# Kernel optimization log

Hardware: AMD Instinct MI355X
Metric: run time of the kernel (lower is better)

The kernel has to match this reference:

```python
import jax, jax.numpy as jnp
import numpy as np

N_NODES = 100000
N_EDGES = 1600000
HID = 128
N_CONV = 3  # num_layers - 1
OUT_DIM = 1
BN_EPS = 1e-5


def _batchnorm(z, gamma, beta):
    # training-mode BN over node dim (batch statistics, biased variance)
    mean = jnp.mean(z, axis=0)
    var = jnp.mean((z - mean) ** 2, axis=0)
    return (z - mean) * jax.lax.rsqrt(var + BN_EPS) * gamma + beta


def setup_inputs() -> dict:
    key = jax.random.key(0)
    ks = jax.random.split(key, 16)
    s = 0.05
    inp = {
        "x": jax.random.randint(ks[0], (N_NODES,), 0, 2, dtype=jnp.int32),
        "edge_index": jax.random.randint(ks[1], (2, N_EDGES), 0, N_NODES, dtype=jnp.int64),
        "emb": jax.random.normal(ks[2], (2, HID), jnp.float32) * s,
        "W1": jax.random.normal(ks[3], (N_CONV, HID, HID), jnp.float32) * s,
        "W2": jax.random.normal(ks[4], (N_CONV, HID, HID), jnp.float32) * s,
        "bn1_g": jnp.ones((N_CONV, HID), jnp.float32),
        "bn1_b": jnp.zeros((N_CONV, HID), jnp.float32),
        "bn2_g": jnp.ones((N_CONV, HID), jnp.float32),
        "bn2_b": jnp.zeros((N_CONV, HID), jnp.float32),
        "rW1": jax.random.normal(ks[5], (4 * HID, HID), jnp.float32) * s,
        "rb1": jnp.zeros((HID,), jnp.float32),
        "rW2": jax.random.normal(ks[6], (HID, OUT_DIM), jnp.float32) * s,
        "rb2": jnp.zeros((OUT_DIM,), jnp.float32),
    }
    return inp


def reference(x, edge_index, emb, W1, W2, bn1_g, bn1_b, bn2_g, bn2_b, rW1, rb1, rW2, rb2):
    n = x.shape[0]
    src, dst = edge_index[0], edge_index[1]
    h = emb[x]  # [N, HID]
    reps = [h]
    for i in range(N_CONV):
        # GINConv: mlp((1+eps)*h + sum_{j in N(i)} h_j), eps=0
        agg = jax.ops.segment_sum(h[src], dst, num_segments=n)
        z = h + agg
        z = jnp.einsum('nd,df->nf', z, W1[i])
        z = jax.nn.relu(_batchnorm(z, bn1_g[i], bn1_b[i]))
        z = jnp.einsum('nd,df->nf', z, W2[i])
        z = _batchnorm(z, bn2_g[i], bn2_b[i])  # PyG BatchNorm after conv
        h = jax.nn.elu(z)
        reps.append(h)
    cat = jnp.concatenate(reps, axis=-1)  # [N, 4*HID]
    hid = jax.nn.relu(cat @ rW1 + rb1)
    return hid @ rW2 + rb2  # [N, OUT_DIM]
```

## Files before the change

kernel.cpp:

```cpp
#include <hip/hip_runtime.h>
#include <hip/hip_fp16.h>
#include <cstdint>
#include <cstddef>

#define NN 100000
#define NE 1600000
#define HID 128
#define BN_EPS 1e-5f
#define NB_SCAN 98
#define BM 96
#define NBLK ((NN + BM - 1) / BM)
#define NBC  ((NN + 255) / 256)
#define SA 72
#define SC_CHUNKS 256
#define SC_RANGE (NN / 8)
#define SC_EPC (NE / SC_CHUNKS)

typedef __attribute__((ext_vector_type(8))) short bf16x8;
typedef __attribute__((ext_vector_type(8))) _Float16 f16x8;
typedef __attribute__((ext_vector_type(4))) float f32x4;
typedef __attribute__((ext_vector_type(4))) unsigned short u16x4;

static constexpr size_t SZ_NODE = (size_t)NN * HID * 4;
static constexpr size_t SZ_H16  = (size_t)NN * HID * 2;
static constexpr size_t OFF_P   = 0;
static constexpr size_t OFF_Q   = SZ_NODE;
static constexpr size_t OFF_R   = 2 * SZ_NODE;
static constexpr size_t OFF_CSR = 3 * SZ_NODE;
static constexpr size_t OFF_RP  = OFF_CSR + (size_t)NE * 4;
static constexpr size_t OFF_ZZ  = ((OFF_RP + (size_t)(NN + 1) * 4 + 255) / 256) * 256;
static constexpr size_t OFF_CNT = OFF_ZZ;
static constexpr size_t OFF_BS  = OFF_CNT + (((size_t)NN * 4 + 255) / 256) * 256;
static constexpr size_t OFF_FLG = OFF_BS + 512;
static constexpr size_t OFF_SS  = OFF_FLG + 256;
static constexpr size_t OFF_SCT = OFF_SS + 5 * 256 * 4;
static constexpr size_t ZZ_END  = ((OFF_SCT + 5 * 4 + 255) / 256) * 256;
static constexpr size_t ZZ_BYTES = ZZ_END - OFF_ZZ;
static constexpr size_t OFF_AC  = ZZ_END;
static constexpr size_t OFF_E   = OFF_AC + 6 * 256 * 4;
static constexpr size_t OFF_WSP = OFF_E + 512 * 4;
static constexpr size_t WS_NEEDED = OFF_WSP + (size_t)8 * 2 * HID * HID * 2;

__device__ __forceinline__ unsigned short f2bf(float f) {
  unsigned u = __float_as_uint(f);
  unsigned r = (u + 0x7fffu + ((u >> 16) & 1u)) >> 16;
  return (unsigned short)r;
}
__device__ __forceinline__ float bf2f(unsigned short b) {
  return __uint_as_float(((unsigned)b) << 16);
}
__device__ __forceinline__ int edge_at(const int* __restrict__ E, int f, int idx) {
  return f ? E[2 * (long long)idx] : E[idx];
}

__global__ void k_detect(const int* __restrict__ E, int* __restrict__ flag) {
  if (threadIdx.x == 0 && blockIdx.x == 0) {
    int f = 1;
    for (int i = 1; i < 256; i += 2)
      if (E[i] != 0) { f = 0; break; }
    *flag = f;
  }
}

__global__ __launch_bounds__(256) void k_hist(const int* __restrict__ E,
                                              const int* __restrict__ flag,
                                              int* __restrict__ cnt) {
  const int f = *flag;
  const int r = blockIdx.x & 7;
  const int chunk = blockIdx.x >> 3;
  const int lo = r * SC_RANGE, hi = lo + SC_RANGE;
  const int ebeg = chunk * SC_EPC, eend = ebeg + SC_EPC;
  for (int e = ebeg + threadIdx.x; e < eend; e += 256) {
    int d = edge_at(E, f, NE + e);
    d = min(max(d, 0), NN - 1);
    if (d >= lo && d < hi) atomicAdd(&cnt[d], 1);
  }
}

__global__ __launch_bounds__(256) void k_scan1(const int* __restrict__ cnt,
                                               int* __restrict__ rp,
                                               int* __restrict__ bs) {
  __shared__ int s[256];
  const int tid = threadIdx.x;
  const int base = blockIdx.x * 1024 + tid * 4;
  int v0 = 0, v1 = 0, v2 = 0, v3 = 0;
  if (base + 0 < NN) v0 = cnt[base + 0];
  if (base + 1 < NN) v1 = cnt[base + 1];
  if (base + 2 < NN) v2 = cnt[base + 2];
  if (base + 3 < NN) v3 = cnt[base + 3];
  const int t0 = v0, t1 = t0 + v1, t2 = t1 + v2, t3 = t2 + v3;
  s[tid] = t3;
  __syncthreads();
  for (int off = 1; off < 256; off <<= 1) {
    int xv = 0;
    if (tid >= off) xv = s[tid - off];
    __syncthreads();
    if (tid >= off) s[tid] += xv;
    __syncthreads();
  }
  const int excl = tid ? s[tid - 1] : 0;
  if (base + 0 < NN) rp[base + 0] = excl;
  if (base + 1 < NN) rp[base + 1] = excl + t0;
  if (base + 2 < NN) rp[base + 2] = excl + t1;
  if (base + 3 < NN) rp[base + 3] = excl + t2;
  if (tid == 255) bs[blockIdx.x] = s[255];
}

__global__ __launch_bounds__(128) void k_scan2(int* __restrict__ bs) {
  __shared__ int s[128];
  const int tid = threadIdx.x;
  s[tid] = (tid < NB_SCAN) ? bs[tid] : 0;
  __syncthreads();
  for (int off = 1; off < 128; off <<= 1) {
    int xv = 0;
    if (tid >= off) xv = s[tid - off];
    __syncthreads();
    if (tid >= off) s[tid] += xv;
    __syncthreads();
  }
  if (tid < NB_SCAN) bs[tid] = tid ? s[tid - 1] : 0;
}

__global__ __launch_bounds__(256) void k_scan3(int* __restrict__ rp,
                                               const int* __restrict__ bs,
                                               int* __restrict__ cursor) {
  const int off = bs[blockIdx.x];
  const int base = blockIdx.x * 1024 + threadIdx.x * 4;
  #pragma unroll
  for (int j = 0; j < 4; ++j) {
    const int i = base + j;
    if (i < NN) {
      const int v = rp[i] + off;
      rp[i] = v;
      cursor[i] = v;
    }
  }
  if (blockIdx.x == 0 && threadIdx.x == 0) rp[NN] = NE;
}

__global__ __launch_bounds__(256) void k_scatter(const int* __restrict__ E,
                                                 const int* __restrict__ flag,
                                                 const int* __restrict__ x,
                                                 int* __restrict__ cursor,
                                                 int* __restrict__ csr) {
  const int f = *flag;
  const int r = blockIdx.x & 7;
  const int chunk = blockIdx.x >> 3;
  const int lo = r * SC_RANGE, hi = lo + SC_RANGE;
  const int ebeg = chunk * SC_EPC, eend = ebeg + SC_EPC;
  for (int e = ebeg + threadIdx.x; e < eend; e += 256) {
    int d = edge_at(E, f, NE + e);
    d = min(max(d, 0), NN - 1);
    if (d >= lo && d < hi) {
      int s = edge_at(E, f, e);
      s = min(max(s, 0), NN - 1);
      const int xb = x[s] & 1;
      const int pos = atomicAdd(&cursor[d], 1);
      if ((unsigned)pos < (unsigned)NE) csr[pos] = s | (xb << 31);
    }
  }
}

__global__ __launch_bounds__(256) void k_prepw(const float* __restrict__ W1,
                                               const float* __restrict__ W2,
                                               const float* __restrict__ rW1,
                                               short* __restrict__ wsp) {
  const int g = blockIdx.x * 256 + threadIdx.x;
  const int m = g >> 14, idx = g & 16383;
  const int k = idx >> 7, n = idx & 127;
  const float* src;
  switch (m) {
    case 0: src = W2; break;
    case 1: src = W1 + 1 * HID * HID; break;
    case 2: src = W2 + 1 * HID * HID; break;
    case 3: src = W1 + 2 * HID * HID; break;
    case 4: src = W2 + 2 * HID * HID; break;
    case 5: src = rW1 + 1 * HID * HID; break;
    case 6: src = rW1 + 2 * HID * HID; break;
    default: src = rW1 + 3 * HID * HID; break;
  }
  const float v = src[k * HID + n];
  short* dst = wsp + (size_t)m * 32768;
  if (m < 5) {
    const unsigned short hb = f2bf(v);
    dst[n * HID + k] = (short)hb;
    dst[16384 + n * HID + k] = (short)f2bf(v - bf2f(hb));
  } else {
    const __half hh = __float2half_rn(v);
    const float rem = v - __half2float(hh);
    const __half hl = __float2half_rn(rem * 2048.f);
    dst[n * HID + k] = (short)__half_as_ushort(hh);
    dst[16384 + n * HID + k] = (short)__half_as_ushort(hl);
  }
}

__global__ __launch_bounds__(256) void k_prep(const float* __restrict__ emb,
                                              const float* __restrict__ W1,
                                              const float* __restrict__ rW1,
                                              float* __restrict__ ee) {
  const int t = threadIdx.x;
  const int f = t & 127;
  const float* er = emb + (t >> 7) * HID;
  float se = 0.f, sr = 0.f;
  for (int k = 0; k < HID; ++k) {
    const float ev = er[k];
    se = fmaf(ev, W1[k * HID + f], se);
    sr = fmaf(ev, rW1[k * HID + f], sr);
  }
  ee[t] = se;
  ee[256 + t] = sr;
}

__global__ __launch_bounds__(256) void k_cnt(const int* __restrict__ x,
                                             const int* __restrict__ rp,
                                             const int* __restrict__ csr,
                                             int* __restrict__ a01,
                                             float* __restrict__ momp) {
  const int n = blockIdx.x * 256 + threadIdx.x;
  float m[5] = {0.f, 0.f, 0.f, 0.f, 0.f};
  if (n < NN) {
    const int beg = rp[n], end = rp[n + 1];
    int c1 = 0;
    for (int j = beg; j < end; ++j) c1 += (int)(((unsigned)csr[j]) >> 31);
    const int a1 = c1 + (x[n] & 1);
    const int a0 = (end - beg + 1) - a1;
    a01[n] = a0 | (a1 << 16);
    m[0] = (float)a0;
    m[1] = (float)a1;
    m[2] = (float)a0 * (float)a0;
    m[3] = (float)a1 * (float)a1;
    m[4] = (float)a0 * (float)a1;
  }
  #pragma unroll
  for (int j = 0; j < 5; ++j)
    #pragma unroll
    for (int off = 1; off < 64; off <<= 1) m[j] += __shfl_xor(m[j], off);
  __shared__ float sm[5][4];
  const int lane = threadIdx.x & 63, wv = threadIdx.x >> 6;
  if (lane == 0)
    #pragma unroll
    for (int j = 0; j < 5; ++j) sm[j][wv] = m[j];
  __syncthreads();
  if (threadIdx.x == 0)
    #pragma unroll
    for (int j = 0; j < 5; ++j)
      momp[j * NBC + blockIdx.x] = sm[j][0] + sm[j][1] + sm[j][2] + sm[j][3];
}

__global__ __launch_bounds__(128) void k_bnmom(const float* __restrict__ momp,
                                               const float* __restrict__ ee,
                                               const float* __restrict__ g,
                                               const float* __restrict__ b,
                                               float* __restrict__ a,
                                               float* __restrict__ c) {
  __shared__ float red[5][128];
  const int t = threadIdx.x;
  float s[5] = {0.f, 0.f, 0.f, 0.f, 0.f};
  for (int i = t; i < NBC; i += 128)
    #pragma unroll
    for (int j = 0; j < 5; ++j) s[j] += momp[j * NBC + i];
  #pragma unroll
  for (int j = 0; j < 5; ++j) red[j][t] = s[j];
  __syncthreads();
  for (int off = 64; off; off >>= 1) {
    if (t < off)
      #pragma unroll
      for (int j = 0; j < 5; ++j) red[j][t] += red[j][t + off];
    __syncthreads();
  }
  const float S0 = red[0][0], S1 = red[1][0];
  const float S00 = red[2][0], S11 = red[3][0], S01 = red[4][0];
  const float inv_n = 1.0f / (float)NN;
  const float e0 = ee[t], e1 = ee[128 + t];
  const float mean = (S0 * e0 + S1 * e1) * inv_n;
  const float msq = (S00 * e0 * e0 + 2.f * S01 * e0 * e1 + S11 * e1 * e1) * inv_n;
  float var = fmaxf(msq - mean * mean, 0.f);
  const float rs = rsqrtf(var + BN_EPS);
  const float av = g[t] * rs;
  a[t] = av;
  c[t] = b[t] - mean * av;
}

__global__ __launch_bounds__(256) void k_agg(const __half* __restrict__ h,
                                             const int* __restrict__ rp,
                                             const int* __restrict__ csr,
                                             float* __restrict__ z) {
  const int wid = blockIdx.x * 4 + (threadIdx.x >> 6);
  const int lane = threadIdx.x & 63;
  if (wid >= NN) return;
  const int beg = rp[wid], end = rp[wid + 1];
  float2 acc = __half22float2(*((const __half2*)(h + (size_t)wid * HID) + lane));
  for (int j = beg; j < end; j += 64) {
    const int cnt = min(64, end - j);
    int idx = (lane < cnt) ? (csr[j + lane] & 0x7fffffff) : 0;
    idx = min(idx, NN - 1);
    int k = 0;
    for (; k + 4 <= cnt; k += 4) {
      const int s0 = __shfl(idx, k + 0), s1 = __shfl(idx, k + 1);
      const int s2 = __shfl(idx, k + 2), s3 = __shfl(idx, k + 3);
      const float2 v0 = __half22float2(*((const __half2*)(h + (size_t)s0 * HID) + lane));
      const float2 v1 = __half22float2(*((const __half2*)(h + (size_t)s1 * HID) + lane));
      const float2 v2 = __half22float2(*((const __half2*)(h + (size_t)s2 * HID) + lane));
      const float2 v3 = __half22float2(*((const __half2*)(h + (size_t)s3 * HID) + lane));
      acc.x += (v0.x + v1.x) + (v2.x + v3.x);
      acc.y += (v0.y + v1.y) + (v2.y + v3.y);
    }
    for (; k < cnt; ++k) {
      const int s = __shfl(idx, k);
      const float2 v = __half22float2(*((const __half2*)(h + (size_t)s * HID) + lane));
      acc.x += v.x;
      acc.y += v.y;
    }
  }
  *(float2*)(z + (size_t)wid * HID + lane * 2) = acc;
}

template <int IN_ACT, int OUT_MODE>
__global__ __launch_bounds__(256, 4) void k_gemm(
    float* A, const short* __restrict__ Wsp,
    const float* __restrict__ ina, const float* __restrict__ inc,
    float* __restrict__ out, float* __restrict__ part,
    const int* __restrict__ a01, const float* __restrict__ ee) {
  __shared__ short Ah[BM * SA];
  __shared__ short Al[BM * SA];
  const int tid = threadIdx.x;
  const int lane = tid & 63, wv = tid >> 6;
  const int tq = lane >> 4, tl = lane & 15;
  const int wc = wv * 32;
  const int m0 = blockIdx.x * BM;

  f32x4 acc[6][2];
  #pragma unroll
  for (int i = 0; i < 6; ++i)
    #pragma unroll
    for (int j = 0; j < 2; ++j) acc[i][j] = (f32x4)(0.f);

  for (int kt = 0; kt < HID; kt += 64) {
    if (kt) __syncthreads();
    #pragma unroll
    for (int p = 0; p < 6; ++p) {
      const int flat = p * 256 + tid;
      const int m = flat >> 4, kq = flat & 15;
      const int gm = m0 + m, gk = kt + kq * 4;
      float vv[4] = {0.f, 0.f, 0.f, 0.f};
      if (gm < NN) {
        if (IN_ACT == 2) {
          const int pk = a01[gm];
          const float a0 = (float)(pk & 0xffff), a1 = (float)(pk >> 16);
          const float4 e0q = *(const float4*)(ee + gk);
          const float4 e1q = *(const float4*)(ee + 128 + gk);
          vv[0] = a0 * e0q.x + a1 * e1q.x;
          vv[1] = a0 * e0q.y + a1 * e1q.y;
          vv[2] = a0 * e0q.z + a1 * e1q.z;
          vv[3] = a0 * e0q.w + a1 * e1q.w;
        } else {
          const float4 v = *(const float4*)(A + (size_t)gm * HID + gk);
          vv[0] = v.x; vv[1] = v.y; vv[2] = v.z; vv[3] = v.w;
        }
        if (IN_ACT >= 1) {
          const float4 a4 = *(const float4*)(ina + gk);
          const float4 c4 = *(const float4*)(inc + gk);
          vv[0] = fmaxf(fmaf(vv[0], a4.x, c4.x), 0.f);
          vv[1] = fmaxf(fmaf(vv[1], a4.y, c4.y), 0.f);
          vv[2] = fmaxf(fmaf(vv[2], a4.z, c4.z), 0.f);
          vv[3] = fmaxf(fmaf(vv[3], a4.w, c4.w), 0.f);
        }
      }
      u16x4 hh, ll;
      #pragma unroll
      for (int j = 0; j < 4; ++j) {
        const unsigned short hb = f2bf(vv[j]);
        hh[j] = hb;
        ll[j] = f2bf(vv[j] - bf2f(hb));
      }
      *(u16x4*)(&Ah[m * SA + kq * 4]) = hh;
      *(u16x4*)(&Al[m * SA + kq * 4]) = ll;
    }
    __syncthreads();
    #pragma unroll
    for (int kc = 0; kc < 64; kc += 32) {
      const int lo = kc + tq * 8;
      const int go = kt + lo;
      bf16x8 wh[2], wl[2];
      #pragma unroll
      for (int fn = 0; fn < 2; ++fn) {
        const int n = wc + fn * 16 + tl;
        wh[fn] = *(const bf16x8*)(Wsp + n * HID + go);
        wl[fn] = *(const bf16x8*)(Wsp + 16384 + n * HID + go);
      }
      #pragma unroll
      for (int fm = 0; fm < 6; ++fm) {
        const int r = (fm * 16 + tl) * SA + lo;
        const bf16x8 ah = *(const bf16x8*)(&Ah[r]);
        const bf16x8 al = *(const bf16x8*)(&Al[r]);
        #pragma unroll
        for (int fn = 0; fn < 2; ++fn) {
          acc[fm][fn] = __builtin_amdgcn_mfma_f32_16x16x32_bf16(ah, wh[fn], acc[fm][fn], 0, 0, 0);
          acc[fm][fn] = __builtin_amdgcn_mfma_f32_16x16x32_bf16(ah, wl[fn], acc[fm][fn], 0, 0, 0);
          acc[fm][fn] = __builtin_amdgcn_mfma_f32_16x16x32_bf16(al, wh[fn], acc[fm][fn], 0, 0, 0);
        }
      }
    }
  }

  #pragma unroll
  for (int fm = 0; fm < 6; ++fm) {
    #pragma unroll
    for (int reg = 0; reg < 4; ++reg) {
      const int row = m0 + fm * 16 + tq * 4 + reg;
      if (row < NN) {
        float* op = out + (size_t)row * HID + wc + tl;
        op[0] = acc[fm][0][reg];
        op[16] = acc[fm][1][reg];
      }
    }
  }
  if (OUT_MODE == 0) {
    #pragma unroll
    for (int fn = 0; fn < 2; ++fn) {
      float s = 0.f, q = 0.f;
      #pragma unroll
      for (int fm = 0; fm < 6; ++fm)
        #pragma unroll
        for (int reg = 0; reg < 4; ++reg) {
          const float v = acc[fm][fn][reg];
          s += v;
          q = fmaf(v, v, q);
        }
      s += __shfl_xor(s, 16); q += __shfl_xor(q, 16);
      s += __shfl_xor(s, 32); q += __shfl_xor(q, 32);
      if (lane < 16) {
        const int col = wc + fn * 16 + lane;
        part[(size_t)blockIdx.x * 256 + col] = s;
        part[(size_t)blockIdx.x * 256 + 128 + col] = q;
      }
    }
  }
}

__global__ __launch_bounds__(256, 3) void k_rdgemm(
    const __half* __restrict__ h1, const __half* __restrict__ h2,
    const __half* __restrict__ h3, const short* __restrict__ wsp,
    const int* __restrict__ x, const float* __restrict__ ee,
    const float* __restrict__ rb1, const float* __restrict__ rW2,
    const float* __restrict__ rb2, float* __restrict__ out) {
  __shared__ short Ah[BM * SA];
  const int tid = threadIdx.x;
  const int lane = tid & 63, wv = tid >> 6;
  const int tq = lane >> 4, tl = lane & 15;
  const int wc = wv * 32;
  const int m0 = blockIdx.x * BM;

  f32x4 ach[6][2], acl[6][2];
  #pragma unroll
  for (int i = 0; i < 6; ++i)
    #pragma unroll
    for (int j = 0; j < 2; ++j) { ach[i][j] = (f32x4)(0.f); acl[i][j] = (f32x4)(0.f); }

  for (int t6 = 0; t6 < 6; ++t6) {
    const __half* hsrc = (t6 < 2) ? h1 : (t6 < 4) ? h2 : h3;
    const short* Ws = wsp + (size_t)(t6 >> 1) * 32768;
    const int kt = (t6 & 1) * 64;
    if (t6) __syncthreads();
    #pragma unroll
    for (int p = 0; p < 6; ++p) {
      const int flat = p * 256 + tid;
      const int m = flat >> 4, kq = flat & 15;
      const int gm = m0 + m, gk = kt + kq * 4;
      u16x4 hv = (u16x4)(0);
      if (gm < NN) hv = *(const u16x4*)((const unsigned short*)hsrc + (size_t)gm * HID + gk);
      *(u16x4*)(&Ah[m * SA + kq * 4]) = hv;
    }
    __syncthreads();
    #pragma unroll
    for (int kc = 0; kc < 64; kc += 32) {
      const int lo = kc + tq * 8;
      const int go = kt + lo;
      f16x8 wh[2], wl[2];
      #pragma unroll
      for (int fn = 0; fn < 2; ++fn) {
        const int n = wc + fn * 16 + tl;
        wh[fn] = *(const f16x8*)(Ws + n * HID + go);
        wl[fn] = *(const f16x8*)(Ws + 16384 + n * HID + go);
      }
      #pragma unroll
      for (int fm = 0; fm < 6; ++fm) {
        const f16x8 a = *(const f16x8*)(&Ah[(fm * 16 + tl) * SA + lo]);
        #pragma unroll
        for (int fn = 0; fn < 2; ++fn) {
          ach[fm][fn] = __builtin_amdgcn_mfma_f32_16x16x32_f16(a, wh[fn], ach[fm][fn], 0, 0, 0);
          acl[fm][fn] = __builtin_amdgcn_mfma_f32_16x16x32_f16(a, wl[fn], acl[fm][fn], 0, 0, 0);
        }
      }
    }
  }

  const int c0 = wc + tl, c1 = wc + 16 + tl;
  const float rb_0 = rb1[c0], rb_1 = rb1[c1];
  const float w2_0 = rW2[c0], w2_1 = rW2[c1];
  const float r0_0 = ee[256 + c0], r0_1 = ee[256 + c1];
  const float r1_0 = ee[384 + c0], r1_1 = ee[384 + c1];
  const float LS = 1.0f / 2048.0f;
  __syncthreads();
  float* rs = (float*)Ah;
  #pragma unroll
  for (int fm = 0; fm < 6; ++fm) {
    #pragma unroll
    for (int reg = 0; reg < 4; ++reg) {
      const int row = fm * 16 + tq * 4 + reg;
      const int grow = m0 + row;
      const int xv = (grow < NN) ? (x[grow] & 1) : 0;
      const float g0 = ach[fm][0][reg] + acl[fm][0][reg] * LS + rb_0 + (xv ? r1_0 : r0_0);
      const float g1 = ach[fm][1][reg] + acl[fm][1][reg] * LS + rb_1 + (xv ? r1_1 : r0_1);
      float p = fmaxf(g0, 0.f) * w2_0 + fmaxf(g1, 0.f) * w2_1;
      p += __shfl_xor(p, 1);
      p += __shfl_xor(p, 2);
      p += __shfl_xor(p, 4);
      p += __shfl_xor(p, 8);
      if (tl == 0) rs[row * 4 + wv] = p;
    }
  }
  __syncthreads();
  if (tid < BM) {
    const int grow = m0 + tid;
    if (grow < NN)
      out[grow] = rs[tid * 4 + 0] + rs[tid * 4 + 1] + rs[tid * 4 + 2] +
                  rs[tid * 4 + 3] + rb2[0];
  }
}

__global__ __launch_bounds__(256) void k_bnstat(const float* __restrict__ part,
                                                const float* __restrict__ g,
                                                const float* __restrict__ b,
                                                float* __restrict__ a,
                                                float* __restrict__ c,
                                                float* __restrict__ S,
                                                int* __restrict__ ctr) {
  const int tid = threadIdx.x;
  float acc = 0.f;
  for (int r = blockIdx.x; r < NBLK; r += 64) acc += part[(size_t)r * 256 + tid];
  atomicAdd(&S[tid], acc);
  __syncthreads();
  __threadfence();
  __shared__ int last;
  if (tid == 0) last = (atomicAdd(ctr, 1) == 63);
  __syncthreads();
  if (!last) return;
  __threadfence();
  const float tot = atomicAdd(&S[tid], 0.f);
  __shared__ float sm[256];
  sm[tid] = tot;
  __syncthreads();
  if (tid < 128) {
    const float inv_n = 1.0f / (float)NN;
    const float mean = sm[tid] * inv_n;
    float var = fmaxf(sm[tid + 128] * inv_n - mean * mean, 0.f);
    const float rs = rsqrtf(var + BN_EPS);
    const float av = g[tid] * rs;
    a[tid] = av;
    c[tid] = b[tid] - mean * av;
  }
}

__global__ __launch_bounds__(256) void k_act(const float* __restrict__ v,
                                             const float* __restrict__ a,
                                             const float* __restrict__ c,
                                             __half* __restrict__ h) {
  const int total = NN * 32;
  for (int i = blockIdx.x * blockDim.x + threadIdx.x; i < total;
       i += gridDim.x * blockDim.x) {
    const int node = i >> 5, q = i & 31;
    const float4 vv = *(const float4*)(v + (size_t)node * HID + q * 4);
    const float4 a4 = ((const float4*)a)[q];
    const float4 c4 = ((const float4*)c)[q];
    float z;
    float o0, o1, o2, o3;
    z = fmaf(vv.x, a4.x, c4.x); o0 = z > 0.f ? z : expm1f(z);
    z = fmaf(vv.y, a4.y, c4.y); o1 = z > 0.f ? z : expm1f(z);
    z = fmaf(vv.z, a4.z, c4.z); o2 = z > 0.f ? z : expm1f(z);
    z = fmaf(vv.w, a4.w, c4.w); o3 = z > 0.f ? z : expm1f(z);
    const __half2 p0 = __floats2half2_rn(o0, o1);
    const __half2 p1 = __floats2half2_rn(o2, o3);
    uint2 u;
    u.x = *reinterpret_cast<const unsigned*>(&p0);
    u.y = *reinterpret_cast<const unsigned*>(&p1);
    *(uint2*)(h + (size_t)node * HID + q * 4) = u;
  }
}

extern "C" void kernel_launch(void* const* d_in, const int* in_sizes, int n_in,
                              void* d_out, int out_size, void* d_ws,
                              size_t ws_size, hipStream_t stream) {
  if (ws_size < WS_NEEDED) return;

  const int* x = (const int*)d_in[0];
  const int* E = (const int*)d_in[1];
  const float* emb = (const float*)d_in[2];
  const float* W1 = (const float*)d_in[3];
  const float* W2 = (const float*)d_in[4];
  const float* bn1g = (const float*)d_in[5];
  const float* bn1b = (const float*)d_in[6];
  const float* bn2g = (const float*)d_in[7];
  const float* bn2b = (const float*)d_in[8];
  const float* rW1 = (const float*)d_in[9];
  const float* rb1 = (const float*)d_in[10];
  const float* rW2 = (const float*)d_in[11];
  const float* rb2 = (const float*)d_in[12];
  float* outp = (float*)d_out;

  char* ws = (char*)d_ws;
  float* P = (float*)(ws + OFF_P);
  float* Q = (float*)(ws + OFF_Q);
  float* R = (float*)(ws + OFF_R);
  int* csr = (int*)(ws + OFF_CSR);
  int* rp = (int*)(ws + OFF_RP);
  int* cnt = (int*)(ws + OFF_CNT);
  int* bs = (int*)(ws + OFF_BS);
  int* flag = (int*)(ws + OFF_FLG);
  float* SS = (float*)(ws + OFF_SS);
  int* SCT = (int*)(ws + OFF_SCT);
  float* ac = (float*)(ws + OFF_AC);
  float* ee = (float*)(ws + OFF_E);
  short* wsp = (short*)(ws + OFF_WSP);
  __half* h1 = (__half*)P;
  __half* h2 = (__half*)((char*)P + SZ_H16);
  __half* h3 = (__half*)R;
  float* part = R;
  int* a01 = (int*)((char*)P + (4 << 20));
  float* momp = (float*)((char*)P + (8 << 20));

  hipMemsetAsync(ws + OFF_ZZ, 0, ZZ_BYTES, stream);
  k_detect<<<1, 64, 0, stream>>>(E, flag);
  k_hist<<<SC_CHUNKS * 8, 256, 0, stream>>>(E, flag, cnt);
  k_scan1<<<NB_SCAN, 256, 0, stream>>>(cnt, rp, bs);
  k_scan2<<<1, 128, 0, stream>>>(bs);
  k_scan3<<<NB_SCAN, 256, 0, stream>>>(rp, bs, cnt);
  k_scatter<<<SC_CHUNKS * 8, 256, 0, stream>>>(E, flag, x, cnt, csr);
  k_prep<<<1, 256, 0, stream>>>(emb, W1, rW1, ee);
  k_prepw<<<512, 256, 0, stream>>>(W1, W2, rW1, wsp);

  float* a1 = ac + 0 * 256, *c1 = a1 + HID;
  float* a2 = ac + 1 * 256, *c2 = a2 + HID;

  k_cnt<<<NBC, 256, 0, stream>>>(x, rp, csr, a01, momp);
  k_bnmom<<<1, 128, 0, stream>>>(momp, ee, bn1g, bn1b, a1, c1);
  k_gemm<2, 0><<<NBLK, 256, 0, stream>>>(Q, wsp + 0 * 32768, a1, c1, Q, part,
                                         a01, ee);
  k_bnstat<<<64, 256, 0, stream>>>(part, bn2g, bn2b, a2, c2, SS + 0 * 256, SCT + 0);
  k_act<<<2048, 256, 0, stream>>>(Q, a2, c2, h1);

  int inst = 1;
  for (int i = 1; i < 3; ++i) {
    float* b1a = ac + (2 * i) * 256, *b1c = b1a + HID;
    float* b2a = ac + (2 * i + 1) * 256, *b2c = b2a + HID;
    const int s1 = (i == 1) ? 1 : 3;
    const __half* hin = (i == 1) ? h1 : h2;
    k_agg<<<NN / 4, 256, 0, stream>>>(hin, rp, csr, Q);
    k_gemm<0, 0><<<NBLK, 256, 0, stream>>>(Q, wsp + (size_t)s1 * 32768,
                                           nullptr, nullptr, Q, part, nullptr,
                                           nullptr);
    k_bnstat<<<64, 256, 0, stream>>>(part, bn1g + i * HID, bn1b + i * HID, b1a,
                                     b1c, SS + inst * 256, SCT + inst);
    ++inst;
    k_gemm<1, 0><<<NBLK, 256, 0, stream>>>(Q, wsp + (size_t)(s1 + 1) * 32768,
                                           b1a, b1c, Q, part, nullptr, nullptr);
    k_bnstat<<<64, 256, 0, stream>>>(part, bn2g + i * HID, bn2b + i * HID, b2a,
                                     b2c, SS + inst * 256, SCT + inst);
    ++inst;
    k_act<<<2048, 256, 0, stream>>>(Q, b2a, b2c, (i == 1) ? h2 : h3);
  }

  k_rdgemm<<<NBLK, 256, 0, stream>>>(h1, h2, h3, wsp + (size_t)5 * 32768, x, ee,
                                     rb1, rW2, rb2, outp);
}
```

Measured before the change: 710.1 us.

## Rewrite GEMMs to load activations straight into registers, dropping LDS staging

The node-level GEMM and readout GEMM kernels are restructured. Each wave now owns 32 rows and all 128 output columns, and reads its A fragments directly from global memory into MFMA registers. This removes the LDS staging and the block-wide barriers. Per-block column statistics are reduced through a small shared buffer. The readout GEMM also drops the low-order fp16 weight correction term and its extra MFMAs, which costs some precision in the final MLP. The trade-off is more weight traffic per wave and lower accuracy in the readout.

New measurement: 819.1 us. 15.3% more time.

```diff
diff --git a/kernel.cpp b/kernel.cpp
--- a/kernel.cpp
+++ b/kernel.cpp
@@ -8,10 +8,9 @@
 #define HID 128
 #define BN_EPS 1e-5f
 #define NB_SCAN 98
-#define BM 96
-#define NBLK ((NN + BM - 1) / BM)
+#define BM2 128
+#define NBLK2 ((NN + BM2 - 1) / BM2)
 #define NBC  ((NN + 255) / 256)
-#define SA 72
 #define SC_CHUNKS 256
 #define SC_RANGE (NN / 8)
 #define SC_EPC (NE / SC_CHUNKS)
@@ -19,7 +18,6 @@
 typedef __attribute__((ext_vector_type(8))) short bf16x8;
 typedef __attribute__((ext_vector_type(8))) _Float16 f16x8;
 typedef __attribute__((ext_vector_type(4))) float f32x4;
-typedef __attribute__((ext_vector_type(4))) unsigned short u16x4;
 
 static constexpr size_t SZ_NODE = (size_t)NN * HID * 4;
 static constexpr size_t SZ_H16  = (size_t)NN * HID * 2;
@@ -187,10 +185,8 @@
     dst[16384 + n * HID + k] = (short)f2bf(v - bf2f(hb));
   } else {
     const __half hh = __float2half_rn(v);
-    const float rem = v - __half2float(hh);
-    const __half hl = __float2half_rn(rem * 2048.f);
     dst[n * HID + k] = (short)__half_as_ushort(hh);
-    dst[16384 + n * HID + k] = (short)__half_as_ushort(hl);
+    dst[16384 + n * HID + k] = 0;
   }
 }
 
@@ -315,217 +311,213 @@
   *(float2*)(z + (size_t)wid * HID + lane * 2) = acc;
 }
 
-template <int IN_ACT, int OUT_MODE>
-__global__ __launch_bounds__(256, 4) void k_gemm(
-    float* A, const short* __restrict__ Wsp,
+template <int IN_ACT>
+__global__ __launch_bounds__(256, 4) void k_gemm2(
+    const float* __restrict__ A, const short* __restrict__ Wsp,
     const float* __restrict__ ina, const float* __restrict__ inc,
     float* __restrict__ out, float* __restrict__ part,
     const int* __restrict__ a01, const float* __restrict__ ee) {
-  __shared__ short Ah[BM * SA];
-  __shared__ short Al[BM * SA];
+  __shared__ float red[4][256];
   const int tid = threadIdx.x;
   const int lane = tid & 63, wv = tid >> 6;
   const int tq = lane >> 4, tl = lane & 15;
-  const int wc = wv * 32;
-  const int m0 = blockIdx.x * BM;
-
-  f32x4 acc[6][2];
-  #pragma unroll
-  for (int i = 0; i < 6; ++i)
-    #pragma unroll
-    for (int j = 0; j < 2; ++j) acc[i][j] = (f32x4)(0.f);
-
-  for (int kt = 0; kt < HID; kt += 64) {
-    if (kt) __syncthreads();
-    #pragma unroll
-    for (int p = 0; p < 6; ++p) {
-      const int flat = p * 256 + tid;
-      const int m = flat >> 4, kq = flat & 15;
-      const int gm = m0 + m, gk = kt + kq * 4;
-      float vv[4] = {0.f, 0.f, 0.f, 0.f};
-      if (gm < NN) {
-        if (IN_ACT == 2) {
-          const int pk = a01[gm];
-          const float a0 = (float)(pk & 0xffff), a1 = (float)(pk >> 16);
-          const float4 e0q = *(const float4*)(ee + gk);
-          const float4 e1q = *(const float4*)(ee + 128 + gk);
-          vv[0] = a0 * e0q.x + a1 * e1q.x;
-          vv[1] = a0 * e0q.y + a1 * e1q.y;
-          vv[2] = a0 * e0q.z + a1 * e1q.z;
-          vv[3] = a0 * e0q.w + a1 * e1q.w;
-        } else {
-          const float4 v = *(const float4*)(A + (size_t)gm * HID + gk);
-          vv[0] = v.x; vv[1] = v.y; vv[2] = v.z; vv[3] = v.w;
-        }
-        if (IN_ACT >= 1) {
-          const float4 a4 = *(const float4*)(ina + gk);
-          const float4 c4 = *(const float4*)(inc + gk);
-          vv[0] = fmaxf(fmaf(vv[0], a4.x, c4.x), 0.f);
-          vv[1] = fmaxf(fmaf(vv[1], a4.y, c4.y), 0.f);
-          vv[2] = fmaxf(fmaf(vv[2], a4.z, c4.z), 0.f);
-          vv[3] = fmaxf(fmaf(vv[3], a4.w, c4.w), 0.f);
-        }
-      }
-      u16x4 hh, ll;
+  const int rw = blockIdx.x * BM2 + wv * 32;
+
+  f32x4 acc[2][8];
+  #pragma unroll
+  for (int i = 0; i < 2; ++i)
+    #pragma unroll
+    for (int j = 0; j < 8; ++j) acc[i][j] = (f32x4)(0.f);
+
+  int a01r[2] = {0, 0};
+  if (IN_ACT == 2) {
+    a01r[0] = a01[min(rw + tl, NN - 1)];
+    a01r[1] = a01[min(rw + 16 + tl, NN - 1)];
+  }
+
+  #pragma unroll
+  for (int ks = 0; ks < 4; ++ks) {
+    const int kg = ks * 32 + tq * 8;
+    float aa[8], cc[8];
+    if (IN_ACT >= 1) {
+      const float4 a0 = *(const float4*)(ina + kg);
+      const float4 a1 = *(const float4*)(ina + kg + 4);
+      const float4 c0 = *(const float4*)(inc + kg);
+      const float4 c1 = *(const float4*)(inc + kg + 4);
+      aa[0] = a0.x; aa[1] = a0.y; aa[2] = a0.z; aa[3] = a0.w;
+      aa[4] = a1.x; aa[5] = a1.y; aa[6] = a1.z; aa[7] = a1.w;
+      cc[0] = c0.x; cc[1] = c0.y; cc[2] = c0.z; cc[3] = c0.w;
+      cc[4] = c1.x; cc[5] = c1.y; cc[6] = c1.z; cc[7] = c1.w;
+    }
+    float e0v[8], e1v[8];
+    if (IN_ACT == 2) {
+      const float4 p0 = *(const float4*)(ee + kg);
+      const float4 p1 = *(const float4*)(ee + kg + 4);
+      const float4 q0 = *(const float4*)(ee + 128 + kg);
+      const float4 q1 = *(const float4*)(ee + 128 + kg + 4);
+      e0v[0] = p0.x; e0v[1] = p0.y; e0v[2] = p0.z; e0v[3] = p0.w;
+      e0v[4] = p1.x; e0v[5] = p1.y; e0v[6] = p1.z; e0v[7] = p1.w;
+      e1v[0] = q0.x; e1v[1] = q0.y; e1v[2] = q0.z; e1v[3] = q0.w;
+      e1v[4] = q1.x; e1v[5] = q1.y; e1v[6] = q1.z; e1v[7] = q1.w;
+    }
+    bf16x8 ah[2], al[2];
+    #pragma unroll
+    for (int fm = 0; fm < 2; ++fm) {
+      const int row = rw + fm * 16 + tl;
+      const int rc = min(row, NN - 1);
+      float vv[8];
+      if (IN_ACT == 2) {
+        const float b0 = (float)(a01r[fm] & 0xffff);
+        const float b1 = (float)(a01r[fm] >> 16);
+        #pragma unroll
+        for (int j = 0; j < 8; ++j) vv[j] = b0 * e0v[j] + b1 * e1v[j];
+      } else {
+        const float4 v0 = *(const float4*)(A + (size_t)rc * HID + kg);
+        const float4 v1 = *(const float4*)(A + (size_t)rc * HID + kg + 4);
+        vv[0] = v0.x; vv[1] = v0.y; vv[2] = v0.z; vv[3] = v0.w;
+        vv[4] = v1.x; vv[5] = v1.y; vv[6] = v1.z; vv[7] = v1.w;
+      }
+      if (IN_ACT >= 1) {
+        #pragma unroll
+        for (int j = 0; j < 8; ++j) vv[j] = fmaxf(fmaf(vv[j], aa[j], cc[j]), 0.f);
+      }
+      if (row >= NN) {
+        #pragma unroll
+        for (int j = 0; j < 8; ++j) vv[j] = 0.f;
+      }
       #pragma unroll
-      for (int j = 0; j < 4; ++j) {
+      for (int j = 0; j < 8; ++j) {
         const unsigned short hb = f2bf(vv[j]);
-        hh[j] = hb;
-        ll[j] = f2bf(vv[j] - bf2f(hb));
-      }
-      *(u16x4*)(&Ah[m * SA + kq * 4]) = hh;
-      *(u16x4*)(&Al[m * SA + kq * 4]) = ll;
-    }
-    __syncthreads();
-    #pragma unroll
-    for (int kc = 0; kc < 64; kc += 32) {
-      const int lo = kc + tq * 8;
-      const int go = kt + lo;
-      bf16x8 wh[2], wl[2];
+        ah[fm][j] = (short)hb;
+        al[fm][j] = (short)f2bf(vv[j] - bf2f(hb));
+      }
+    }
+    #pragma unroll
+    for (int fn = 0; fn < 8; ++fn) {
+      const int n = fn * 16 + tl;
+      const bf16x8 wh = *(const bf16x8*)(Wsp + n * HID + kg);
+      const bf16x8 wl = *(const bf16x8*)(Wsp + 16384 + n * HID + kg);
       #pragma unroll
-      for (int fn = 0; fn < 2; ++fn) {
-        const int n = wc + fn * 16 + tl;
-        wh[fn] = *(const bf16x8*)(Wsp + n * HID + go);
-        wl[fn] = *(const bf16x8*)(Wsp + 16384 + n * HID + go);
-      }
+      for (int fm = 0; fm < 2; ++fm) {
+        acc[fm][fn] = __builtin_amdgcn_mfma_f32_16x16x32_bf16(ah[fm], wh, acc[fm][fn], 0, 0, 0);
+        acc[fm][fn] = __builtin_amdgcn_mfma_f32_16x16x32_bf16(ah[fm], wl, acc[fm][fn], 0, 0, 0);
+        acc[fm][fn] = __builtin_amdgcn_mfma_f32_16x16x32_bf16(al[fm], wh, acc[fm][fn], 0, 0, 0);
+      }
+    }
+  }
+
+  #pragma unroll
+  for (int fm = 0; fm < 2; ++fm) {
+    #pragma unroll
+    for (int reg = 0; reg < 4; ++reg) {
+      const int row = rw + fm * 16 + tq * 4 + reg;
+      if (row < NN) {
+        float* op = out + (size_t)row * HID + tl;
+        #pragma unroll
+        for (int fn = 0; fn < 8; ++fn) op[fn * 16] = acc[fm][fn][reg];
+      }
+    }
+  }
+  float cs[8], cq[8];
+  #pragma unroll
+  for (int fn = 0; fn < 8; ++fn) {
+    float s = 0.f, q = 0.f;
+    #pragma unroll
+    for (int fm = 0; fm < 2; ++fm)
       #pragma unroll
-      for (int fm = 0; fm < 6; ++fm) {
-        const int r = (fm * 16 + tl) * SA + lo;
-        const bf16x8 ah = *(const bf16x8*)(&Ah[r]);
-        const bf16x8 al = *(const bf16x8*)(&Al[r]);
-        #pragma unroll
-        for (int fn = 0; fn < 2; ++fn) {
-          acc[fm][fn] = __builtin_amdgcn_mfma_f32_16x16x32_bf16(ah, wh[fn], acc[fm][fn], 0, 0, 0);
-          acc[fm][fn] = __builtin_amdgcn_mfma_f32_16x16x32_bf16(ah, wl[fn], acc[fm][fn], 0, 0, 0);
-          acc[fm][fn] = __builtin_amdgcn_mfma_f32_16x16x32_bf16(al, wh[fn], acc[fm][fn], 0, 0, 0);
-        }
-      }
-    }
-  }
-
-  #pragma unroll
-  for (int fm = 0; fm < 6; ++fm) {
-    #pragma unroll
-    for (int reg = 0; reg < 4; ++reg) {
-      const int row = m0 + fm * 16 + tq * 4 + reg;
-      if (row < NN) {
-        float* op = out + (size_t)row * HID + wc + tl;
-        op[0] = acc[fm][0][reg];
-        op[16] = acc[fm][1][reg];
-      }
-    }
-  }
-  if (OUT_MODE == 0) {
-    #pragma unroll
-    for (int fn = 0; fn < 2; ++fn) {
-      float s = 0.f, q = 0.f;
-      #pragma unroll
-      for (int fm = 0; fm < 6; ++fm)
-        #pragma unroll
-        for (int reg = 0; reg < 4; ++reg) {
-          const float v = acc[fm][fn][reg];
-          s += v;
-          q = fmaf(v, v, q);
-        }
-      s += __shfl_xor(s, 16); q += __shfl_xor(q, 16);
-      s += __shfl_xor(s, 32); q += __shfl_xor(q, 32);
-      if (lane < 16) {
-        const int col = wc + fn * 16 + lane;
-        part[(size_t)blockIdx.x * 256 + col] = s;
-        part[(size_t)blockIdx.x * 256 + 128 + col] = q;
-      }
-    }
-  }
-}
-
-__global__ __launch_bounds__(256, 3) void k_rdgemm(
+      for (int reg = 0; reg < 4; ++reg) {
+        const float v = acc[fm][fn][reg];
+        s += v;
+        q = fmaf(v, v, q);
+      }
+    cs[fn] = s;
+    cq[fn] = q;
+  }
+  #pragma unroll
+  for (int fn = 0; fn < 8; ++fn) {
+    cs[fn] += __shfl_xor(cs[fn], 16); cq[fn] += __shfl_xor(cq[fn], 16);
+    cs[fn] += __shfl_xor(cs[fn], 32); cq[fn] += __shfl_xor(cq[fn], 32);
+  }
+  if (lane < 16) {
+    #pragma unroll
+    for (int fn = 0; fn < 8; ++fn) {
+      red[wv][fn * 16 + tl] = cs[fn];
+      red[wv][128 + fn * 16 + tl] = cq[fn];
+    }
+  }
+  __syncthreads();
+  part[(size_t)blockIdx.x * 256 + tid] =
+      red[0][tid] + red[1][tid] + red[2][tid] + red[3][tid];
+}
+
+__global__ __launch_bounds__(256, 4) void k_rdgemm2(
     const __half* __restrict__ h1, const __half* __restrict__ h2,
     const __half* __restrict__ h3, const short* __restrict__ wsp,
     const int* __restrict__ x, const float* __restrict__ ee,
     const float* __restrict__ rb1, const float* __restrict__ rW2,
     const float* __restrict__ rb2, float* __restrict__ out) {
-  __shared__ short Ah[BM * SA];
   const int tid = threadIdx.x;
   const int lane = tid & 63, wv = tid >> 6;
   const int tq = lane >> 4, tl = lane & 15;
-  const int wc = wv * 32;
-  const int m0 = blockIdx.x * BM;
-
-  f32x4 ach[6][2], acl[6][2];
-  #pragma unroll
-  for (int i = 0; i < 6; ++i)
-    #pragma unroll
-    for (int j = 0; j < 2; ++j) { ach[i][j] = (f32x4)(0.f); acl[i][j] = (f32x4)(0.f); }
-
+  const int rw = blockIdx.x * BM2 + wv * 32;
+
+  f32x4 acc[2][8];
+  #pragma unroll
+  for (int i = 0; i < 2; ++i)
+    #pragma unroll
+    for (int j = 0; j < 8; ++j) acc[i][j] = (f32x4)(0.f);
+
+  const int rc0 = min(rw + tl, NN - 1);
+  const int rc1 = min(rw + 16 + tl, NN - 1);
+
+  #pragma unroll
   for (int t6 = 0; t6 < 6; ++t6) {
     const __half* hsrc = (t6 < 2) ? h1 : (t6 < 4) ? h2 : h3;
     const short* Ws = wsp + (size_t)(t6 >> 1) * 32768;
     const int kt = (t6 & 1) * 64;
-    if (t6) __syncthreads();
-    #pragma unroll
-    for (int p = 0; p < 6; ++p) {
-      const int flat = p * 256 + tid;
-      const int m = flat >> 4, kq = flat & 15;
-      const int gm = m0 + m, gk = kt + kq * 4;
-      u16x4 hv = (u16x4)(0);
-      if (gm < NN) hv = *(const u16x4*)((const unsigned short*)hsrc + (size_t)gm * HID + gk);
-      *(u16x4*)(&Ah[m * SA + kq * 4]) = hv;
-    }
-    __syncthreads();
-    #pragma unroll
-    for (int kc = 0; kc < 64; kc += 32) {
-      const int lo = kc + tq * 8;
-      const int go = kt + lo;
-      f16x8 wh[2], wl[2];
+    #pragma unroll
+    for (int kc = 0; kc < 2; ++kc) {
+      const int kg = kt + kc * 32 + tq * 8;
+      f16x8 a[2];
+      a[0] = *(const f16x8*)((const _Float16*)hsrc + (size_t)rc0 * HID + kg);
+      a[1] = *(const f16x8*)((const _Float16*)hsrc + (size_t)rc1 * HID + kg);
       #pragma unroll
-      for (int fn = 0; fn < 2; ++fn) {
-        const int n = wc + fn * 16 + tl;
-        wh[fn] = *(const f16x8*)(Ws + n * HID + go);
-        wl[fn] = *(const f16x8*)(Ws + 16384 + n * HID + go);
-      }
+      for (int fn = 0; fn < 8; ++fn) {
+        const f16x8 wh = *(const f16x8*)(Ws + (fn * 16 + tl) * HID + kg);
+        acc[0][fn] = __builtin_amdgcn_mfma_f32_16x16x32_f16(a[0], wh, acc[0][fn], 0, 0, 0);
+        acc[1][fn] = __builtin_amdgcn_mfma_f32_16x16x32_f16(a[1], wh, acc[1][fn], 0, 0, 0);
+      }
+    }
+  }
+
+  float rbv[8], w2v[8], r0v[8], r1v[8];
+  #pragma unroll
+  for (int fn = 0; fn < 8; ++fn) {
+    const int col = fn * 16 + tl;
+    rbv[fn] = rb1[col];
+    w2v[fn] = rW2[col];
+    r0v[fn] = ee[256 + col];
+    r1v[fn] = ee[384 + col];
+  }
+  const float b2 = rb2[0];
+  #pragma unroll
+  for (int fm = 0; fm < 2; ++fm) {
+    #pragma unroll
+    for (int reg = 0; reg < 4; ++reg) {
+      const int row = rw + fm * 16 + tq * 4 + reg;
+      const int xv = x[min(row, NN - 1)] & 1;
+      float p = 0.f;
       #pragma unroll
-      for (int fm = 0; fm < 6; ++fm) {
-        const f16x8 a = *(const f16x8*)(&Ah[(fm * 16 + tl) * SA + lo]);
-        #pragma unroll
-        for (int fn = 0; fn < 2; ++fn) {
-          ach[fm][fn] = __builtin_amdgcn_mfma_f32_16x16x32_f16(a, wh[fn], ach[fm][fn], 0, 0, 0);
-          acl[fm][fn] = __builtin_amdgcn_mfma_f32_16x16x32_f16(a, wl[fn], acl[fm][fn], 0, 0, 0);
-        }
-      }
-    }
-  }
-
-  const int c0 = wc + tl, c1 = wc + 16 + tl;
-  const float rb_0 = rb1[c0], rb_1 = rb1[c1];
-  const float w2_0 = rW2[c0], w2_1 = rW2[c1];
-  const float r0_0 = ee[256 + c0], r0_1 = ee[256 + c1];
-  const float r1_0 = ee[384 + c0], r1_1 = ee[384 + c1];
-  const float LS = 1.0f / 2048.0f;
-  __syncthreads();
-  float* rs = (float*)Ah;
-  #pragma unroll
-  for (int fm = 0; fm < 6; ++fm) {
-    #pragma unroll
-    for (int reg = 0; reg < 4; ++reg) {
-      const int row = fm * 16 + tq * 4 + reg;
-      const int grow = m0 + row;
-      const int xv = (grow < NN) ? (x[grow] & 1) : 0;
-      const float g0 = ach[fm][0][reg] + acl[fm][0][reg] * LS + rb_0 + (xv ? r1_0 : r0_0);
-      const float g1 = ach[fm][1][reg] + acl[fm][1][reg] * LS + rb_1 + (xv ? r1_1 : r0_1);
-      float p = fmaxf(g0, 0.f) * w2_0 + fmaxf(g1, 0.f) * w2_1;
+      for (int fn = 0; fn < 8; ++fn) {
+        const float g = acc[fm][fn][reg] + rbv[fn] + (xv ? r1v[fn] : r0v[fn]);
+        p = fmaf(fmaxf(g, 0.f), w2v[fn], p);
+      }
       p += __shfl_xor(p, 1);
       p += __shfl_xor(p, 2);
       p += __shfl_xor(p, 4);
       p += __shfl_xor(p, 8);
-      if (tl == 0) rs[row * 4 + wv] = p;
-    }
-  }
-  __syncthreads();
-  if (tid < BM) {
-    const int grow = m0 + tid;
-    if (grow < NN)
-      out[grow] = rs[tid * 4 + 0] + rs[tid * 4 + 1] + rs[tid * 4 + 2] +
-                  rs[tid * 4 + 3] + rb2[0];
+      if (tl == 0 && row < NN) out[row] = p + b2;
+    }
   }
 }
 
@@ -538,7 +530,7 @@
                                                 int* __restrict__ ctr) {
   const int tid = threadIdx.x;
   float acc = 0.f;
-  for (int r = blockIdx.x; r < NBLK; r += 64) acc += part[(size_t)r * 256 + tid];
+  for (int r = blockIdx.x; r < NBLK2; r += 64) acc += part[(size_t)r * 256 + tid];
   atomicAdd(&S[tid], acc);
   __syncthreads();
   __threadfence();
@@ -644,8 +636,8 @@
 
   k_cnt<<<NBC, 256, 0, stream>>>(x, rp, csr, a01, momp);
   k_bnmom<<<1, 128, 0, stream>>>(momp, ee, bn1g, bn1b, a1, c1);
-  k_gemm<2, 0><<<NBLK, 256, 0, stream>>>(Q, wsp + 0 * 32768, a1, c1, Q, part,
-                                         a01, ee);
+  k_gemm2<2><<<NBLK2, 256, 0, stream>>>(Q, wsp + 0 * 32768, a1, c1, Q, part,
+                                        a01, ee);
   k_bnstat<<<64, 256, 0, stream>>>(part, bn2g, bn2b, a2, c2, SS + 0 * 256, SCT + 0);
   k_act<<<2048, 256, 0, stream>>>(Q, a2, c2, h1);
 
@@ -656,20 +648,19 @@
     const int s1 = (i == 1) ? 1 : 3;
     const __half* hin = (i == 1) ? h1 : h2;
     k_agg<<<NN / 4, 256, 0, stream>>>(hin, rp, csr, Q);
-    k_gemm<0, 0><<<NBLK, 256, 0, stream>>>(Q, wsp + (size_t)s1 * 32768,
-                                           nullptr, nullptr, Q, part, nullptr,
-                                           nullptr);
+    k_gemm2<0><<<NBLK2, 256, 0, stream>>>(Q, wsp + (size_t)s1 * 32768, nullptr,
+                                          nullptr, Q, part, nullptr, nullptr);
     k_bnstat<<<64, 256, 0, stream>>>(part, bn1g + i * HID, bn1b + i * HID, b1a,
                                      b1c, SS + inst * 256, SCT + inst);
     ++inst;
-    k_gemm<1, 0><<<NBLK, 256, 0, stream>>>(Q, wsp + (size_t)(s1 + 1) * 32768,
-                                           b1a, b1c, Q, part, nullptr, nullptr);
+    k_gemm2<1><<<NBLK2, 256, 0, stream>>>(Q, wsp + (size_t)(s1 + 1) * 32768,
+                                          b1a, b1c, Q, part, nullptr, nullptr);
     k_bnstat<<<64, 256, 0, stream>>>(part, bn2g + i * HID, bn2b + i * HID, b2a,
                                      b2c, SS + inst * 256, SCT + inst);
     ++inst;
     k_act<<<2048, 256, 0, stream>>>(Q, b2a, b2c, (i == 1) ? h2 : h3);
   }
 
-  k_rdgemm<<<NBLK, 256, 0, stream>>>(h1, h2, h3, wsp + (size_t)5 * 32768, x, ee,
-                                     rb1, rW2, rb2, outp);
-}
+  k_rdgemm2<<<NBLK2, 256, 0, stream>>>(h1, h2, h3, wsp + (size_t)5 * 32768, x,
+                                       ee, rb1, rW2, rb2, outp);
+}
```
